# Kernel optimization log

Measured on AMD Instinct MI355X. Metric: run time of the kernel, lower is better.

The kernel has to match this reference:

```python
import jax, jax.numpy as jnp
import numpy as np

NUM_HEADS = 8
EMBED_DIM = 64
HEAD_DIM = EMBED_DIM // NUM_HEADS
B, N, T = 2, 512, 24


def setup_inputs() -> dict:
    key = jax.random.key(0)
    ks = jax.random.split(key, 8)
    shp = (B, N, T, EMBED_DIM)
    return {
        "values": jax.random.normal(ks[0], shp, jnp.float32),
        "keys": jax.random.normal(ks[1], shp, jnp.float32),
        "query": jax.random.normal(ks[2], shp, jnp.float32),
        "Wv": jax.random.normal(ks[3], (HEAD_DIM, HEAD_DIM), jnp.float32) / np.sqrt(HEAD_DIM),
        "Wk": jax.random.normal(ks[4], (HEAD_DIM, HEAD_DIM), jnp.float32) / np.sqrt(HEAD_DIM),
        "Wq": jax.random.normal(ks[5], (HEAD_DIM, HEAD_DIM), jnp.float32) / np.sqrt(HEAD_DIM),
        "Wo": jax.random.normal(ks[6], (EMBED_DIM, EMBED_DIM), jnp.float32) / np.sqrt(EMBED_DIM),
        "bo": jnp.zeros((EMBED_DIM,), jnp.float32),
    }


def reference(values, keys, query, Wv, Wk, Wq, Wo, bo):
    b, n, t, e = query.shape
    h, d = NUM_HEADS, HEAD_DIM
    # split heads: (b, n, t, h, d)
    v = values.reshape(b, n, t, h, d) @ Wv.T
    k = keys.reshape(b, n, t, h, d) @ Wk.T
    q = query.reshape(b, n, t, h, d) @ Wq.T
    # node-axis attention per (timestep, head)
    energy = jnp.einsum('bqthd,bkthd->bqkth', q, k)  # (b, q_nodes, k_nodes, t, h)
    attn = jax.nn.softmax(energy / jnp.sqrt(jnp.float32(e)), axis=2)
    out = jnp.einsum('bqkth,bkthd->bqthd', attn, v).reshape(b, n, t, h * d)
    return out @ Wo.T + bo
```

## Files before the change

### kernel.cpp

```cpp
#include <hip/hip_runtime.h>

#define NUM_HEADS 8
#define EMBED 64
#define BB 2
#define NN 512
#define TT 24

typedef _Float16 half4v __attribute__((ext_vector_type(4)));
typedef _Float16 half2v __attribute__((ext_vector_type(2)));
typedef __fp16   fp16x2 __attribute__((ext_vector_type(2)));
typedef __fp16   fp16x4 __attribute__((ext_vector_type(4)));
typedef float    f32x4  __attribute__((ext_vector_type(4)));

#define KSTRIDE 20
#define VSTRIDE 524

__global__ __launch_bounds__(256) void attn_kernel(
    const float* __restrict__ values,
    const float* __restrict__ keys,
    const float* __restrict__ query,
    const float* __restrict__ Wv,
    const float* __restrict__ Wk,
    const float* __restrict__ Wq,
    float* __restrict__ out)
{
    __shared__ float w[192];
    __shared__ __align__(16) _Float16 Kpad[NN * KSTRIDE];
    __shared__ __align__(16) _Float16 Qpad[256 * KSTRIDE];
    __shared__ __align__(16) _Float16 Vt[16 * VSTRIDE];

    const int tid  = threadIdx.x;
    const int half = blockIdx.x >= 384;
    const int grp  = blockIdx.x - half * 384;
    const int h = grp & 7;
    const int t = (grp >> 3) % TT;
    const int b = grp / (8 * TT);

    if (tid < 192) {
        float v;
        if (tid < 64)       v = Wq[tid];
        else if (tid < 128) v = Wk[tid - 64];
        else                v = Wv[tid - 128];
        w[tid] = v;
    }
    {
        unsigned int* z = (unsigned int*)(Vt + 8 * VSTRIDE);
        for (int i = tid; i < 8 * VSTRIDE / 2; i += 256) z[i] = 0u;
    }
    __syncthreads();

    {
        const int r0 = 2 * tid;
        const long base0 = ((long)(b * NN + r0) * TT + t) * EMBED + h * 8;
        const long base1 = base0 + (long)TT * EMBED;
        float4 ka0 = *(const float4*)(keys + base0);
        float4 ka1 = *(const float4*)(keys + base0 + 4);
        float4 kb0 = *(const float4*)(keys + base1);
        float4 kb1 = *(const float4*)(keys + base1 + 4);
        float4 va0 = *(const float4*)(values + base0);
        float4 va1 = *(const float4*)(values + base0 + 4);
        float4 vb0 = *(const float4*)(values + base1);
        float4 vb1 = *(const float4*)(values + base1 + 4);
        float k0[8] = {ka0.x, ka0.y, ka0.z, ka0.w, ka1.x, ka1.y, ka1.z, ka1.w};
        float k1[8] = {kb0.x, kb0.y, kb0.z, kb0.w, kb1.x, kb1.y, kb1.z, kb1.w};
        float v0[8] = {va0.x, va0.y, va0.z, va0.w, va1.x, va1.y, va1.z, va1.w};
        float v1[8] = {vb0.x, vb0.y, vb0.z, vb0.w, vb1.x, vb1.y, vb1.z, vb1.w};
        half4v klo0, khi0, klo1, khi1;
        #pragma unroll
        for (int dp = 0; dp < 8; ++dp) {
            float sk0 = 0.f, sk1 = 0.f, sv0 = 0.f, sv1 = 0.f;
            #pragma unroll
            for (int d = 0; d < 8; ++d) {
                const float wk = w[64 + dp * 8 + d], wvv = w[128 + dp * 8 + d];
                sk0 += k0[d] * wk;  sk1 += k1[d] * wk;
                sv0 += v0[d] * wvv; sv1 += v1[d] * wvv;
            }
            if (dp < 4) { klo0[dp] = (_Float16)sk0; klo1[dp] = (_Float16)sk1; }
            else        { khi0[dp - 4] = (_Float16)sk0; khi1[dp - 4] = (_Float16)sk1; }
            half2v vv = {(_Float16)sv0, (_Float16)sv1};
            *(half2v*)(Vt + dp * VSTRIDE + r0) = vv;
        }
        const half4v zz = {(_Float16)0.f, (_Float16)0.f, (_Float16)0.f, (_Float16)0.f};
        *(half4v*)(Kpad + r0 * KSTRIDE)            = klo0;
        *(half4v*)(Kpad + r0 * KSTRIDE + 4)        = khi0;
        *(half4v*)(Kpad + r0 * KSTRIDE + 8)        = zz;
        *(half4v*)(Kpad + r0 * KSTRIDE + 12)       = zz;
        *(half4v*)(Kpad + (r0 + 1) * KSTRIDE)      = klo1;
        *(half4v*)(Kpad + (r0 + 1) * KSTRIDE + 4)  = khi1;
        *(half4v*)(Kpad + (r0 + 1) * KSTRIDE + 8)  = zz;
        *(half4v*)(Kpad + (r0 + 1) * KSTRIDE + 12) = zz;

        const long qbase = ((long)(b * NN + half * 256 + tid) * TT + t) * EMBED + h * 8;
        float4 q0 = *(const float4*)(query + qbase);
        float4 q1 = *(const float4*)(query + qbase + 4);
        float qx[8] = {q0.x, q0.y, q0.z, q0.w, q1.x, q1.y, q1.z, q1.w};
        const float scale = 0.125f * 1.44269504088896340736f;
        half4v qlo, qhi;
        #pragma unroll
        for (int dp = 0; dp < 8; ++dp) {
            float s = 0.f;
            #pragma unroll
            for (int d = 0; d < 8; ++d) s += qx[d] * w[dp * 8 + d];
            s *= scale;
            if (dp < 4) qlo[dp] = (_Float16)s; else qhi[dp - 4] = (_Float16)s;
        }
        *(half4v*)(Qpad + tid * KSTRIDE)      = qlo;
        *(half4v*)(Qpad + tid * KSTRIDE + 4)  = qhi;
        *(half4v*)(Qpad + tid * KSTRIDE + 8)  = zz;
        *(half4v*)(Qpad + tid * KSTRIDE + 12) = zz;
    }
    __syncthreads();

    const int wv   = tid >> 6;
    const int lane = tid & 63;
    const int ln   = lane & 15;
    const int quad = lane >> 4;

    #pragma unroll 1
    for (int pass = 0; pass < 4; ++pass) {
        const int ql0 = pass * 64 + wv * 16;
        const half4v Qf = *(const half4v*)(Qpad + (ql0 + ln) * KSTRIDE + quad * 4);
        f32x4 O = {0.f, 0.f, 0.f, 0.f};
        float l0 = 0.f, l1 = 0.f, l2 = 0.f, l3 = 0.f;
        const f32x4 zero4 = {0.f, 0.f, 0.f, 0.f};
        #pragma unroll 4
        for (int kt = 0; kt < 32; ++kt) {
            half4v Kf = *(const half4v*)(Kpad + (kt * 16 + ln) * KSTRIDE + quad * 4);
            f32x4 E = __builtin_amdgcn_mfma_f32_16x16x16f16(Kf, Qf, zero4, 0, 0, 0);
            float p0 = __builtin_amdgcn_exp2f(E[0]);
            float p1 = __builtin_amdgcn_exp2f(E[1]);
            float p2 = __builtin_amdgcn_exp2f(E[2]);
            float p3 = __builtin_amdgcn_exp2f(E[3]);
            l0 += p0; l1 += p1; l2 += p2; l3 += p3;
            fp16x2 plo = __builtin_amdgcn_cvt_pkrtz(p0, p1);
            fp16x2 phi = __builtin_amdgcn_cvt_pkrtz(p2, p3);
            half4v Pf = __builtin_bit_cast(half4v,
                (fp16x4)__builtin_shufflevector(plo, phi, 0, 1, 2, 3));
            half4v Vf = *(const half4v*)(Vt + ln * VSTRIDE + kt * 16 + quad * 4);
            O = __builtin_amdgcn_mfma_f32_16x16x16f16(Vf, Pf, O, 0, 0, 0);
        }
        float l = (l0 + l1) + (l2 + l3);
        l += __shfl_xor(l, 16, 64);
        l += __shfl_xor(l, 32, 64);
        const float inv = 1.0f / l;
        if (lane < 32) {
            const long obase = ((long)(b * NN + half * 256 + ql0 + ln) * TT + t) * EMBED
                             + h * 8 + quad * 4;
            float4 o = make_float4(O[0] * inv, O[1] * inv, O[2] * inv, O[3] * inv);
            *(float4*)(out + obase) = o;
        }
    }
}

#define PSTRIDE 68
__global__ __launch_bounds__(256) void proj_kernel(
    const float* __restrict__ Wo,
    const float* __restrict__ bo,
    float* __restrict__ io)
{
    __shared__ float As[64 * PSTRIDE];
    __shared__ float WsT[64 * PSTRIDE];
    __shared__ float bos[EMBED];

    const int tid = threadIdx.x;
    const int row0 = blockIdx.x * 64;

    {
        const int r = tid >> 2;
        const int seg = tid & 3;
        #pragma unroll
        for (int i = 0; i < 4; ++i) {
            const int c = seg * 16 + i * 4;
            float4 av = *(const float4*)(io + (long)(row0 + r) * 64 + c);
            *(float4*)(As + r * PSTRIDE + c) = av;
        }
        #pragma unroll
        for (int i = 0; i < 16; ++i) {
            const int idx = tid + i * 256;
            WsT[(idx & 63) * PSTRIDE + (idx >> 6)] = Wo[idx];
        }
        if (tid < 64) bos[tid] = bo[tid];
    }
    __syncthreads();

    const int rg = tid >> 4;
    const int cg = tid & 15;
    float c[4][4] = {};
    #pragma unroll
    for (int kq = 0; kq < 16; ++kq) {
        float4 a[4], wt[4];
        #pragma unroll
        for (int i = 0; i < 4; ++i)
            a[i] = *(const float4*)(As + (rg * 4 + i) * PSTRIDE + kq * 4);
        #pragma unroll
        for (int kk = 0; kk < 4; ++kk)
            wt[kk] = *(const float4*)(WsT + (kq * 4 + kk) * PSTRIDE + cg * 4);
        #pragma unroll
        for (int kk = 0; kk < 4; ++kk) {
            const float aa[4] = {a[0].x, a[1].x, a[2].x, a[3].x};
            (void)aa;
        }
        #pragma unroll
        for (int i = 0; i < 4; ++i) {
            const float a0 = (i == 0) ? 0.f : 0.f; (void)a0;
            c[i][0] += a[i].x * wt[0].x + a[i].y * wt[1].x + a[i].z * wt[2].x + a[i].w * wt[3].x;
            c[i][1] += a[i].x * wt[0].y + a[i].y * wt[1].y + a[i].z * wt[2].y + a[i].w * wt[3].y;
            c[i][2] += a[i].x * wt[0].z + a[i].y * wt[1].z + a[i].z * wt[2].z + a[i].w * wt[3].z;
            c[i][3] += a[i].x * wt[0].w + a[i].y * wt[1].w + a[i].z * wt[2].w + a[i].w * wt[3].w;
        }
    }
    #pragma unroll
    for (int i = 0; i < 4; ++i) {
        float4 o = make_float4(c[i][0] + bos[cg * 4 + 0],
                               c[i][1] + bos[cg * 4 + 1],
                               c[i][2] + bos[cg * 4 + 2],
                               c[i][3] + bos[cg * 4 + 3]);
        *(float4*)(io + (long)(row0 + rg * 4 + i) * 64 + cg * 4) = o;
    }
}

extern "C" void kernel_launch(void* const* d_in, const int* in_sizes, int n_in,
                              void* d_out, int out_size, void* d_ws, size_t ws_size,
                              hipStream_t stream) {
    const float* values = (const float*)d_in[0];
    const float* keys   = (const float*)d_in[1];
    const float* query  = (const float*)d_in[2];
    const float* Wv     = (const float*)d_in[3];
    const float* Wk     = (const float*)d_in[4];
    const float* Wq     = (const float*)d_in[5];
    const float* Wo     = (const float*)d_in[6];
    const float* bo     = (const float*)d_in[7];
    float* out = (float*)d_out;

    (void)in_sizes; (void)n_in; (void)out_size; (void)d_ws; (void)ws_size;

    attn_kernel<<<BB * TT * NUM_HEADS * 2, 256, 0, stream>>>(
        values, keys, query, Wv, Wk, Wq, out);
    proj_kernel<<<(BB * NN * TT) / 64, 256, 0, stream>>>(Wo, bo, out);
}
```

Baseline: 118.5 us.

## Fold softmax row-sum into MFMA via ones row in V, process two query tiles

The padding row 8 of the transposed V tile is filled with fp16 ones, so the PV MFMA also produces the softmax denominator and the per-lane exp sum accumulation and cross-lane reductions go away; the denominator is read back with a single shuffle. Each wave now handles two 16-query tiles per pass, sharing K and V fragment loads across two MFMA chains for more instruction-level parallelism. Global loads of K, V and Q are hoisted above the weight-staging barrier to overlap their latency. The denominator is now summed from fp16-rounded probabilities, which slightly changes numerics, and the extra live accumulators add register pressure.

Result: no change. 116.4 us (-1.8%).

```diff
diff --git a/kernel.cpp b/kernel.cpp
--- a/kernel.cpp
+++ b/kernel.cpp
@@ -36,6 +36,21 @@
     const int t = (grp >> 3) % TT;
     const int b = grp / (8 * TT);
 
+    const int r0 = 2 * tid;
+    const long base0 = ((long)(b * NN + r0) * TT + t) * EMBED + h * 8;
+    const long base1 = base0 + (long)TT * EMBED;
+    const long qbase = ((long)(b * NN + half * 256 + tid) * TT + t) * EMBED + h * 8;
+    float4 ka0 = *(const float4*)(keys + base0);
+    float4 ka1 = *(const float4*)(keys + base0 + 4);
+    float4 kb0 = *(const float4*)(keys + base1);
+    float4 kb1 = *(const float4*)(keys + base1 + 4);
+    float4 va0 = *(const float4*)(values + base0);
+    float4 va1 = *(const float4*)(values + base0 + 4);
+    float4 vb0 = *(const float4*)(values + base1);
+    float4 vb1 = *(const float4*)(values + base1 + 4);
+    float4 q0 = *(const float4*)(query + qbase);
+    float4 q1 = *(const float4*)(query + qbase + 4);
+
     if (tid < 192) {
         float v;
         if (tid < 64)       v = Wq[tid];
@@ -45,22 +60,12 @@
     }
     {
         unsigned int* z = (unsigned int*)(Vt + 8 * VSTRIDE);
-        for (int i = tid; i < 8 * VSTRIDE / 2; i += 256) z[i] = 0u;
+        for (int i = tid; i < 8 * VSTRIDE / 2; i += 256)
+            z[i] = (i < VSTRIDE / 2) ? 0x3C003C00u : 0u;
     }
     __syncthreads();
 
     {
-        const int r0 = 2 * tid;
-        const long base0 = ((long)(b * NN + r0) * TT + t) * EMBED + h * 8;
-        const long base1 = base0 + (long)TT * EMBED;
-        float4 ka0 = *(const float4*)(keys + base0);
-        float4 ka1 = *(const float4*)(keys + base0 + 4);
-        float4 kb0 = *(const float4*)(keys + base1);
-        float4 kb1 = *(const float4*)(keys + base1 + 4);
-        float4 va0 = *(const float4*)(values + base0);
-        float4 va1 = *(const float4*)(values + base0 + 4);
-        float4 vb0 = *(const float4*)(values + base1);
-        float4 vb1 = *(const float4*)(values + base1 + 4);
         float k0[8] = {ka0.x, ka0.y, ka0.z, ka0.w, ka1.x, ka1.y, ka1.z, ka1.w};
         float k1[8] = {kb0.x, kb0.y, kb0.z, kb0.w, kb1.x, kb1.y, kb1.z, kb1.w};
         float v0[8] = {va0.x, va0.y, va0.z, va0.w, va1.x, va1.y, va1.z, va1.w};
@@ -90,9 +95,6 @@
         *(half4v*)(Kpad + (r0 + 1) * KSTRIDE + 8)  = zz;
         *(half4v*)(Kpad + (r0 + 1) * KSTRIDE + 12) = zz;
 
-        const long qbase = ((long)(b * NN + half * 256 + tid) * TT + t) * EMBED + h * 8;
-        float4 q0 = *(const float4*)(query + qbase);
-        float4 q1 = *(const float4*)(query + qbase + 4);
         float qx[8] = {q0.x, q0.y, q0.z, q0.w, q1.x, q1.y, q1.z, q1.w};
         const float scale = 0.125f * 1.44269504088896340736f;
         half4v qlo, qhi;
@@ -115,39 +117,47 @@
     const int lane = tid & 63;
     const int ln   = lane & 15;
     const int quad = lane >> 4;
+    const f32x4 zero4 = {0.f, 0.f, 0.f, 0.f};
 
     #pragma unroll 1
-    for (int pass = 0; pass < 4; ++pass) {
-        const int ql0 = pass * 64 + wv * 16;
-        const half4v Qf = *(const half4v*)(Qpad + (ql0 + ln) * KSTRIDE + quad * 4);
-        f32x4 O = {0.f, 0.f, 0.f, 0.f};
-        float l0 = 0.f, l1 = 0.f, l2 = 0.f, l3 = 0.f;
-        const f32x4 zero4 = {0.f, 0.f, 0.f, 0.f};
+    for (int pass = 0; pass < 2; ++pass) {
+        const int ql0 = pass * 128 + wv * 32;
+        const half4v Qa = *(const half4v*)(Qpad + (ql0 + ln) * KSTRIDE + quad * 4);
+        const half4v Qb = *(const half4v*)(Qpad + (ql0 + 16 + ln) * KSTRIDE + quad * 4);
+        f32x4 Oa = {0.f, 0.f, 0.f, 0.f};
+        f32x4 Ob = {0.f, 0.f, 0.f, 0.f};
         #pragma unroll 4
         for (int kt = 0; kt < 32; ++kt) {
             half4v Kf = *(const half4v*)(Kpad + (kt * 16 + ln) * KSTRIDE + quad * 4);
-            f32x4 E = __builtin_amdgcn_mfma_f32_16x16x16f16(Kf, Qf, zero4, 0, 0, 0);
-            float p0 = __builtin_amdgcn_exp2f(E[0]);
-            float p1 = __builtin_amdgcn_exp2f(E[1]);
-            float p2 = __builtin_amdgcn_exp2f(E[2]);
-            float p3 = __builtin_amdgcn_exp2f(E[3]);
-            l0 += p0; l1 += p1; l2 += p2; l3 += p3;
-            fp16x2 plo = __builtin_amdgcn_cvt_pkrtz(p0, p1);
-            fp16x2 phi = __builtin_amdgcn_cvt_pkrtz(p2, p3);
-            half4v Pf = __builtin_bit_cast(half4v,
-                (fp16x4)__builtin_shufflevector(plo, phi, 0, 1, 2, 3));
             half4v Vf = *(const half4v*)(Vt + ln * VSTRIDE + kt * 16 + quad * 4);
-            O = __builtin_amdgcn_mfma_f32_16x16x16f16(Vf, Pf, O, 0, 0, 0);
-        }
-        float l = (l0 + l1) + (l2 + l3);
-        l += __shfl_xor(l, 16, 64);
-        l += __shfl_xor(l, 32, 64);
-        const float inv = 1.0f / l;
+            f32x4 Ea = __builtin_amdgcn_mfma_f32_16x16x16f16(Kf, Qa, zero4, 0, 0, 0);
+            f32x4 Eb = __builtin_amdgcn_mfma_f32_16x16x16f16(Kf, Qb, zero4, 0, 0, 0);
+            fp16x2 pa0 = __builtin_amdgcn_cvt_pkrtz(__builtin_amdgcn_exp2f(Ea[0]),
+                                                    __builtin_amdgcn_exp2f(Ea[1]));
+            fp16x2 pa1 = __builtin_amdgcn_cvt_pkrtz(__builtin_amdgcn_exp2f(Ea[2]),
+                                                    __builtin_amdgcn_exp2f(Ea[3]));
+            fp16x2 pb0 = __builtin_amdgcn_cvt_pkrtz(__builtin_amdgcn_exp2f(Eb[0]),
+                                                    __builtin_amdgcn_exp2f(Eb[1]));
+            fp16x2 pb1 = __builtin_amdgcn_cvt_pkrtz(__builtin_amdgcn_exp2f(Eb[2]),
+                                                    __builtin_amdgcn_exp2f(Eb[3]));
+            half4v Pa = __builtin_bit_cast(half4v,
+                (fp16x4)__builtin_shufflevector(pa0, pa1, 0, 1, 2, 3));
+            half4v Pb = __builtin_bit_cast(half4v,
+                (fp16x4)__builtin_shufflevector(pb0, pb1, 0, 1, 2, 3));
+            Oa = __builtin_amdgcn_mfma_f32_16x16x16f16(Vf, Pa, Oa, 0, 0, 0);
+            Ob = __builtin_amdgcn_mfma_f32_16x16x16f16(Vf, Pb, Ob, 0, 0, 0);
+        }
+        const float la = __shfl(Oa[0], 32 + ln, 64);
+        const float lb = __shfl(Ob[0], 32 + ln, 64);
+        const float ia = 1.0f / la;
+        const float ib = 1.0f / lb;
         if (lane < 32) {
-            const long obase = ((long)(b * NN + half * 256 + ql0 + ln) * TT + t) * EMBED
-                             + h * 8 + quad * 4;
-            float4 o = make_float4(O[0] * inv, O[1] * inv, O[2] * inv, O[3] * inv);
-            *(float4*)(out + obase) = o;
+            const long oa = ((long)(b * NN + half * 256 + ql0 + ln) * TT + t) * EMBED
+                          + h * 8 + quad * 4;
+            const long ob = ((long)(b * NN + half * 256 + ql0 + 16 + ln) * TT + t) * EMBED
+                          + h * 8 + quad * 4;
+            *(float4*)(out + oa) = make_float4(Oa[0] * ia, Oa[1] * ia, Oa[2] * ia, Oa[3] * ia);
+            *(float4*)(out + ob) = make_float4(Ob[0] * ib, Ob[1] * ib, Ob[2] * ib, Ob[3] * ib);
         }
     }
 }
@@ -196,13 +206,7 @@
         for (int kk = 0; kk < 4; ++kk)
             wt[kk] = *(const float4*)(WsT + (kq * 4 + kk) * PSTRIDE + cg * 4);
         #pragma unroll
-        for (int kk = 0; kk < 4; ++kk) {
-            const float aa[4] = {a[0].x, a[1].x, a[2].x, a[3].x};
-            (void)aa;
-        }
-        #pragma unroll
         for (int i = 0; i < 4; ++i) {
-            const float a0 = (i == 0) ? 0.f : 0.f; (void)a0;
             c[i][0] += a[i].x * wt[0].x + a[i].y * wt[1].x + a[i].z * wt[2].x + a[i].w * wt[3].x;
             c[i][1] += a[i].x * wt[0].y + a[i].y * wt[1].y + a[i].z * wt[2].y + a[i].w * wt[3].y;
             c[i][2] += a[i].x * wt[0].z + a[i].y * wt[1].z + a[i].z * wt[2].z + a[i].w * wt[3].z;
```
